# Kernel tuning notes

Measured on AMD Instinct MI355X. Metric: run time of the kernel, lower is better.

## Reference

```python
import jax, jax.numpy as jnp
import numpy as np

DIM = 1024
NUM_HEADS = 16
HEAD_DIM = DIM // NUM_HEADS
SCALE = HEAD_DIM ** -0.5
B, N = 4, 2048


def setup_inputs() -> dict:
    key = jax.random.key(0)
    ks = jax.random.split(key, 5)
    s = 1.0 / np.sqrt(DIM)  # ~ torch Linear init scale
    x = jax.random.normal(ks[0], (B, N, DIM), dtype=jnp.float32)
    Wq = jax.random.normal(ks[1], (DIM, DIM), dtype=jnp.float32) * s
    Wk = jax.random.normal(ks[2], (DIM, DIM), dtype=jnp.float32) * s
    Wv = jax.random.normal(ks[3], (DIM, DIM), dtype=jnp.float32) * s
    Wo = jax.random.normal(ks[4], (DIM, DIM), dtype=jnp.float32) * s
    mask = jnp.tril(jnp.ones((N, N), dtype=bool))  # causal 2D bool mask
    return {"x": x, "mask": mask, "Wq": Wq, "Wk": Wk, "Wv": Wv, "Wo": Wo}


def reference(x, mask, Wq, Wk, Wv, Wo):
    Bb, Nn, D = x.shape
    def split_heads(t):
        return t.reshape(Bb, Nn, NUM_HEADS, HEAD_DIM).transpose(0, 2, 1, 3)  # [B,H,N,d]
    q = split_heads(x @ Wq.T)
    k = split_heads(x @ Wk.T)
    v = split_heads(x @ Wv.T)
    attn = jnp.einsum('bhqd,bhkd->bhqk', q, k) * SCALE  # [B,H,N,N]
    # 2D mask -> broadcast over batch and heads; ~mask positions set to -inf
    attn = jnp.where(mask[None, None, :, :], attn, -jnp.inf)
    attn = jax.nn.softmax(attn, axis=-1)
    out = jnp.einsum('bhqk,bhkd->bhqd', attn, v)
    out = out.transpose(0, 2, 1, 3).reshape(Bb, Nn, D)
    return out @ Wo.T
```

## Files before the change

kernel.cpp:

```cpp
#include <hip/hip_runtime.h>
#include <stdint.h>

#define Bq   4
#define Nseq 2048
#define NH   16
#define HD   64
#define DIMD 1024

typedef float  f32x4   __attribute__((ext_vector_type(4)));
typedef float  f32x16  __attribute__((ext_vector_type(16)));
typedef __bf16 bf16x8  __attribute__((ext_vector_type(8)));
typedef short  s16x4   __attribute__((ext_vector_type(4)));

typedef __attribute__((address_space(1))) void as1_void;
typedef __attribute__((address_space(3))) void as3_void;

static __device__ __forceinline__ uint16_t f2bf(float f) {
    uint32_t u = __builtin_bit_cast(uint32_t, f);
    u += 0x7fffu + ((u >> 16) & 1u);
    return (uint16_t)(u >> 16);
}

static __device__ __forceinline__ uint32_t pk2(float a, float b) {
    uint32_t ua = __builtin_bit_cast(uint32_t, a);
    uint32_t ub = __builtin_bit_cast(uint32_t, b);
    return (ua >> 16) | (ub & 0xffff0000u);
}

static __device__ __forceinline__ void asyncLoad16(const uint16_t* g, uint16_t* l) {
    __builtin_amdgcn_global_load_lds((as1_void*)g, (as3_void*)l, 16, 0, 0);
}

__global__ void cast_all(const float* __restrict__ x,
                         const float* __restrict__ wq, const float* __restrict__ wk,
                         const float* __restrict__ wv, const float* __restrict__ wo,
                         uint16_t* __restrict__ dst) {
    size_t i = ((size_t)blockIdx.x * blockDim.x + threadIdx.x) * 4;
    const float* src; size_t off; float scale = 1.0f;
    if (i < 8388608) { src = x; off = i; }
    else {
        size_t wI = i - 8388608;
        size_t wi = wI >> 20;
        off = wI & 1048575;
        src = (wi == 0) ? wq : (wi == 1) ? wk : (wi == 2) ? wv : wo;
        if (wi == 0) scale = 0.18033688011112042f;
    }
    float4 v = *(const float4*)(src + off);
    ushort4 o;
    o.x = f2bf(v.x * scale); o.y = f2bf(v.y * scale);
    o.z = f2bf(v.z * scale); o.w = f2bf(v.w * scale);
    *(ushort4*)(dst + i) = o;
}

#define BARR()  __builtin_amdgcn_s_barrier()
#define SCB0()  __builtin_amdgcn_sched_barrier(0)
#define LGKM()  asm volatile("s_waitcnt lgkmcnt(0)" ::: "memory")
#define PRIO1() __builtin_amdgcn_s_setprio(1)
#define PRIO0() __builtin_amdgcn_s_setprio(0)

__global__ __launch_bounds__(512, 2) void gemm_qkv384(
    const uint16_t* __restrict__ A, const uint16_t* __restrict__ W0,
    uint16_t* __restrict__ C0, uint16_t* __restrict__ vtb)
{
    __shared__ __align__(16) uint16_t Asm[2][2][4096];
    __shared__ __align__(16) uint16_t Bsm[2][2][12288];

    const int t = threadIdx.x, lane = t & 63, w = t >> 6;
    const int wm = w >> 2, wn = w & 3;
    const int ln = lane & 15, l4 = lane >> 4;

    const int m0 = blockIdx.x * 128;
    const int n0 = blockIdx.y * 384;

    const int srow = t >> 3;
    const int sg   = (t & 7) ^ (srow & 7);
    const uint16_t* aBase = A + (size_t)(m0 + (srow >> 5)*64 + (srow & 31))*DIMD + sg*8;
    const uint16_t* bBase[3];
    #pragma unroll
    for (int j = 0; j < 3; ++j) {
        int f = j*64 + srow;
        int wnf = f / 48, off = f % 48;
        bBase[j] = W0 + (size_t)(n0 + wnf*96 + off)*DIMD + sg*8;
    }

#define SA(mh_, buf_, kk_) asyncLoad16(aBase + (size_t)(mh_)*32*DIMD + (kk_), \
        &Asm[buf_][mh_][t*8])
#define SB(nh_, j_, buf_, kk_) asyncLoad16(bBase[j_] + (size_t)(nh_)*48*DIMD + (kk_), \
        &Bsm[buf_][nh_][(j_)*4096 + t*8])

    SA(0,0,0); SA(1,0,0);
    SB(0,0,0,0); SB(0,1,0,0); SB(0,2,0,0);
    SB(1,0,0,0); SB(1,1,0,0); SB(1,2,0,0);
    SA(0,1,64);
    SB(0,0,1,64); SB(0,1,1,64); SB(0,2,1,64);
    asm volatile("s_waitcnt vmcnt(4)" ::: "memory");
    BARR();

    const int cs0 = ( l4      ^ (ln & 7)) * 8;
    const int cs1 = ((4 + l4) ^ (ln & 7)) * 8;
    const int awo = wm*2048 + ln*64;
    const int bwo = wn*3072 + ln*64;

    bf16x8 af[2][2], bf0[3][2], bf1[3][2];
    f32x4 acc[4][6] = {};

#define LDA(mh_, buf_)                                                         \
    _Pragma("unroll")                                                          \
    for (int mf = 0; mf < 2; ++mf) {                                           \
        af[mf][0] = *(const bf16x8*)(&Asm[buf_][mh_][awo + mf*1024 + cs0]);    \
        af[mf][1] = *(const bf16x8*)(&Asm[buf_][mh_][awo + mf*1024 + cs1]);    \
    }
#define LDB(nh_, buf_, BF)                                                     \
    _Pragma("unroll")                                                          \
    for (int nf = 0; nf < 3; ++nf) {                                           \
        BF[nf][0] = *(const bf16x8*)(&Bsm[buf_][nh_][bwo + nf*1024 + cs0]);    \
        BF[nf][1] = *(const bf16x8*)(&Bsm[buf_][nh_][bwo + nf*1024 + cs1]);    \
    }
#define MFMA12(mh_, nh_, BF)                                                   \
    _Pragma("unroll")                                                          \
    for (int mf = 0; mf < 2; ++mf)                                             \
        _Pragma("unroll")                                                      \
        for (int nf = 0; nf < 3; ++nf) {                                       \
            acc[(mh_)*2+mf][(nh_)*3+nf] = __builtin_amdgcn_mfma_f32_16x16x32_bf16( \
                af[mf][0], BF[nf][0], acc[(mh_)*2+mf][(nh_)*3+nf], 0,0,0);     \
            acc[(mh_)*2+mf][(nh_)*3+nf] = __builtin_amdgcn_mfma_f32_16x16x32_bf16( \
                af[mf][1], BF[nf][1], acc[(mh_)*2+mf][(nh_)*3+nf], 0,0,0);     \
        }

    #pragma unroll 1
    for (int i = 0; i < 8; ++i) {
        const int kk1 = i*128 + 64, kk2 = i*128 + 128, kk3 = i*128 + 192;
        const bool pf = (i < 7);

        LDA(0,0); LDB(0,0,bf0);
        SA(1,1,kk1); SB(1,0,1,kk1);
        BARR(); LGKM(); SCB0();
        PRIO1(); MFMA12(0,0,bf0); PRIO0();
        SCB0(); BARR();

        LDB(1,0,bf1);
        SB(1,1,1,kk1); SB(1,2,1,kk1);
        BARR(); LGKM(); SCB0();
        PRIO1(); MFMA12(0,1,bf1); PRIO0();
        SCB0(); BARR();

        LDA(1,0);
        if (pf) { SA(0,0,kk2); SB(0,0,0,kk2); }
        BARR(); LGKM(); SCB0();
        PRIO1(); MFMA12(1,0,bf0); PRIO0();
        SCB0(); BARR();

        if (pf) { SB(0,1,0,kk2); SB(0,2,0,kk2); }
        BARR(); SCB0();
        PRIO1(); MFMA12(1,1,bf1); PRIO0();
        SCB0();
        if (pf) { asm volatile("s_waitcnt vmcnt(4)" ::: "memory"); }
        else    { asm volatile("s_waitcnt vmcnt(0)" ::: "memory"); }
        BARR();

        LDA(0,1); LDB(0,1,bf0);
        if (pf) { SA(1,0,kk2); SB(1,0,0,kk2); }
        BARR(); LGKM(); SCB0();
        PRIO1(); MFMA12(0,0,bf0); PRIO0();
        SCB0(); BARR();

        LDB(1,1,bf1);
        if (pf) { SB(1,1,0,kk2); SB(1,2,0,kk2); }
        BARR(); LGKM(); SCB0();
        PRIO1(); MFMA12(0,1,bf1); PRIO0();
        SCB0(); BARR();

        LDA(1,1);
        if (pf) { SA(0,1,kk3); SB(0,0,1,kk3); }
        BARR(); LGKM(); SCB0();
        PRIO1(); MFMA12(1,0,bf0); PRIO0();
        SCB0(); BARR();

        if (pf) { SB(0,1,1,kk3); SB(0,2,1,kk3); }
        BARR(); SCB0();
        PRIO1(); MFMA12(1,1,bf1); PRIO0();
        SCB0();
        if (pf) { asm volatile("s_waitcnt vmcnt(4)" ::: "memory"); BARR(); }
    }

#undef SA
#undef SB
#undef LDA
#undef LDB
#undef MFMA12

    #pragma unroll
    for (int mh = 0; mh < 2; ++mh)
      #pragma unroll
      for (int mf = 0; mf < 2; ++mf)
        #pragma unroll
        for (int nh = 0; nh < 2; ++nh)
          #pragma unroll
          for (int nf = 0; nf < 3; ++nf) {
              const f32x4 a4 = acc[mh*2+mf][nh*3+nf];
              int rowg = m0 + wm*64 + mh*32 + mf*16 + l4*4;
              int colg = n0 + wn*96 + nh*48 + nf*16 + ln;
              if (colg < 2048) {
                  uint16_t* C = C0 + (size_t)(colg >> 10) * 8388608;
                  int col = colg & 1023;
                  #pragma unroll
                  for (int r = 0; r < 4; ++r)
                      C[(size_t)(rowg + r)*1024 + col] = f2bf(a4[r]);
              } else {
                  int dg = colg - 2048;
                  int bb = rowg >> 11, nn = rowg & 2047;
                  ushort4 o4;
                  o4.x = f2bf(a4[0]); o4.y = f2bf(a4[1]);
                  o4.z = f2bf(a4[2]); o4.w = f2bf(a4[3]);
                  *(ushort4*)(vtb + ((size_t)(bb*1024 + dg))*Nseq + nn) = o4;
              }
          }
}

__global__ __launch_bounds__(512, 2) void gemm_out256(
    const uint16_t* __restrict__ A, const uint16_t* __restrict__ W0,
    float* __restrict__ C)
{
    __shared__ __align__(16) uint16_t Asm[2][2][8192];
    __shared__ __align__(16) uint16_t Bsm[2][2][4096];

    const int t = threadIdx.x, lane = t & 63, w = t >> 6;
    const int wm = w >> 2, wn = w & 3;
    const int ln = lane & 15, l4 = lane >> 4;

    const int m0 = blockIdx.x * 256;
    const int n0 = blockIdx.y * 128;

    const int srow = t >> 3;
    const int sg   = (t & 7) ^ (srow & 7);
    const uint16_t* aBase = A + (size_t)(m0 + srow)*DIMD + sg*8;
    const uint16_t* bBase = W0 + (size_t)(n0 + (srow >> 4)*32 + (srow & 15))*DIMD + sg*8;

#define SA(mh_, j_, buf_, kk_) asyncLoad16(aBase + (size_t)((j_)*128 + (mh_)*64)*DIMD + (kk_), \
        &Asm[buf_][mh_][(j_)*4096 + t*8])
#define SB(nh_, buf_, kk_) asyncLoad16(bBase + (size_t)(nh_)*16*DIMD + (kk_), \
        &Bsm[buf_][nh_][t*8])

    SB(0,0,0); SB(1,0,0);
    SA(0,0,0,0); SA(0,1,0,0);
    SA(1,0,0,0); SA(1,1,0,0);
    SB(0,1,64); SB(1,1,64);
    SA(0,0,1,64); SA(0,1,1,64);
    asm volatile("s_waitcnt vmcnt(4)" ::: "memory");
    BARR();

    const int cs0 = ( l4      ^ (ln & 7)) * 8;
    const int cs1 = ((4 + l4) ^ (ln & 7)) * 8;
    const int awo = wm*4096 + ln*64;
    const int bwo = wn*1024 + ln*64;

    bf16x8 af[4][2], bfA[2], bfB[2];
    f32x4 acc[8][2] = {};

#define LDA(mh_, buf_)                                                         \
    _Pragma("unroll")                                                          \
    for (int mf = 0; mf < 4; ++mf) {                                           \
        af[mf][0] = *(const bf16x8*)(&Asm[buf_][mh_][awo + mf*1024 + cs0]);    \
        af[mf][1] = *(const bf16x8*)(&Asm[buf_][mh_][awo + mf*1024 + cs1]);    \
    }
#define LDB(nh_, buf_, BF)                                                     \
    BF[0] = *(const bf16x8*)(&Bsm[buf_][nh_][bwo + cs0]);                      \
    BF[1] = *(const bf16x8*)(&Bsm[buf_][nh_][bwo + cs1]);
#define MFMA8(mh_, nh_, BF)                                                    \
    _Pragma("unroll")                                                          \
    for (int mf = 0; mf < 4; ++mf) {                                           \
        acc[(mh_)*4+mf][nh_] = __builtin_amdgcn_mfma_f32_16x16x32_bf16(        \
            af[mf][0], BF[0], acc[(mh_)*4+mf][nh_], 0,0,0);                    \
        acc[(mh_)*4+mf][nh_] = __builtin_amdgcn_mfma_f32_16x16x32_bf16(        \
            af[mf][1], BF[1], acc[(mh_)*4+mf][nh_], 0,0,0);                    \
    }

    #pragma unroll 1
    for (int i = 0; i < 8; ++i) {
        const int kk1 = i*128 + 64, kk2 = i*128 + 128, kk3 = i*128 + 192;
        const bool pf2 = (i < 7);
        const bool pf3 = (i < 7);

        LDA(0,0); LDB(0,0,bfA);
        SA(1,0,1,kk1); SA(1,1,1,kk1);
        BARR(); LGKM(); SCB0();
        PRIO1(); MFMA8(0,0,bfA); PRIO0();
        SCB0(); BARR();

        LDB(1,0,bfB);
        BARR(); LGKM(); SCB0();
        PRIO1(); MFMA8(0,1,bfB); PRIO0();
        SCB0(); BARR();

        LDA(1,0);
        if (pf2) { SB(0,0,kk2); SB(1,0,kk2); SA(0,0,0,kk2); SA(0,1,0,kk2); }
        BARR(); LGKM(); SCB0();
        PRIO1(); MFMA8(1,0,bfA); PRIO0();
        SCB0(); BARR();

        BARR(); SCB0();
        PRIO1(); MFMA8(1,1,bfB); PRIO0();
        SCB0();
        if (pf2) { asm volatile("s_waitcnt vmcnt(4)" ::: "memory"); }
        else     { asm volatile("s_waitcnt vmcnt(0)" ::: "memory"); }
        BARR();

        LDA(0,1); LDB(0,1,bfA);
        if (pf2) { SA(1,0,0,kk2); SA(1,1,0,kk2); }
        BARR(); LGKM(); SCB0();
        PRIO1(); MFMA8(0,0,bfA); PRIO0();
        SCB0(); BARR();

        LDB(1,1,bfB);
        BARR(); LGKM(); SCB0();
        PRIO1(); MFMA8(0,1,bfB); PRIO0();
        SCB0(); BARR();

        LDA(1,1);
        if (pf3) { SB(0,1,kk3); SB(1,1,kk3); SA(0,0,1,kk3); SA(0,1,1,kk3); }
        BARR(); LGKM(); SCB0();
        PRIO1(); MFMA8(1,0,bfA); PRIO0();
        SCB0(); BARR();

        BARR(); SCB0();
        PRIO1(); MFMA8(1,1,bfB); PRIO0();
        SCB0();
        if (pf3) { asm volatile("s_waitcnt vmcnt(4)" ::: "memory"); BARR(); }
    }

#undef SA
#undef SB
#undef LDA
#undef LDB
#undef MFMA8

    #pragma unroll
    for (int mh = 0; mh < 2; ++mh)
      #pragma unroll
      for (int mf = 0; mf < 4; ++mf)
        #pragma unroll
        for (int nh = 0; nh < 2; ++nh) {
            const f32x4 a4 = acc[mh*4+mf][nh];
            int rowg = m0 + wm*128 + mh*64 + mf*16 + l4*4;
            int colg = n0 + wn*32 + nh*16 + ln;
            #pragma unroll
            for (int r = 0; r < 4; ++r)
                C[(size_t)(rowg + r)*1024 + colg] = a4[r];
        }
}

__global__ __launch_bounds__(256, 3) void attn(
    const uint16_t* __restrict__ Q, const uint16_t* __restrict__ K,
    const uint16_t* __restrict__ Vt, uint16_t* __restrict__ O)
{
    __shared__ __align__(16) uint16_t Kb[3][64*64];
    __shared__ __align__(16) uint16_t Vb[3][64*64];

    const int t = threadIdx.x, lane = t & 63, w = t >> 6;
    const int quad = lane >> 4, c = lane & 15;
    const int y = blockIdx.y;
    const int qi = (y < 4) ? (15 - y) : (y < 8) ? (y + 4) : (y < 12) ? (y - 4) : (15 - y);
    const int q0 = qi * 128;
    const int bh = blockIdx.x, b = bh >> 4, h = bh & 15;
    const size_t tokBase = (size_t)b * Nseq;
    const int hcol = h * HD;
    uint16_t* Qs = (uint16_t*)Kb;

    #define STAGE_KV(k0_, buf_)                                             \
        _Pragma("unroll")                                                    \
        for (int i = 0; i < 2; ++i) {                                        \
            int s = t + 256*i;                                               \
            int row = s >> 3, gg = (s & 7) ^ (row & 7);                      \
            asyncLoad16(K + (tokBase + (k0_) + row)*DIMD + hcol + gg*8,      \
                        Kb[buf_] + (size_t)(w*64 + 256*i)*8);                \
            asyncLoad16(Vt + ((size_t)bh*HD + row)*Nseq + (k0_) + gg*8,      \
                        Vb[buf_] + (size_t)(w*64 + 256*i)*8);                \
        }

    #pragma unroll
    for (int i = 0; i < 4; ++i) {
        int s = t + 256*i;
        int row = s >> 3, gg = (s & 7) ^ (row & 7);
        asyncLoad16(Q + (tokBase + q0 + row)*DIMD + hcol + gg*8,
                    Qs + (size_t)(w*64 + 256*i)*8);
    }
    __syncthreads();
    bf16x8 qf[2][2];
    #pragma unroll
    for (int qt = 0; qt < 2; ++qt)
        #pragma unroll
        for (int ks = 0; ks < 2; ++ks) {
            int row = w*32 + qt*16 + c;
            int pos = (ks*4 + quad) ^ (row & 7);
            qf[qt][ks] = *(const bf16x8*)(Qs + (size_t)(row*8 + pos)*8);
        }
    __syncthreads();

    const int wrow0 = q0 + w*32;
    const int end = 2*qi + 2;
    STAGE_KV(0, 0);
    STAGE_KV(64, 1);

    f32x4  o[2][4] = {};
    float  l_lane[2] = {0.f, 0.f};
    int b0 = 0, b1 = 1, b2 = 2;

    for (int kt = 0; kt < end; ++kt) {
        const int k0 = kt * 64;

        if (kt + 1 < end) { asm volatile("s_waitcnt vmcnt(4)\n\ts_barrier" ::: "memory"); }
        else              { asm volatile("s_waitcnt vmcnt(0)\n\ts_barrier" ::: "memory"); }

        if (kt + 2 < end) { STAGE_KV((kt+2)*64, b2); }

        if (k0 <= wrow0 + 31) {
            const uint16_t* Ks = Kb[b0];
            const uint16_t* Vs = Vb[b0];

            f32x4 sv[2][4] = {};
            __builtin_amdgcn_s_setprio(1);
            #pragma unroll
            for (int nt = 0; nt < 4; ++nt)
                #pragma unroll
                for (int ks = 0; ks < 2; ++ks) {
                    int row = nt*16 + c;
                    int pos = (ks*4 + quad) ^ (row & 7);
                    bf16x8 kf = *(const bf16x8*)(Ks + (size_t)(row*8 + pos)*8);
                    sv[0][nt] = __builtin_amdgcn_mfma_f32_16x16x32_bf16(kf, qf[0][ks], sv[0][nt], 0, 0, 0);
                    sv[1][nt] = __builtin_amdgcn_mfma_f32_16x16x32_bf16(kf, qf[1][ks], sv[1][nt], 0, 0, 0);
                }
            __builtin_amdgcn_s_setprio(0);

            if (k0 + 63 > wrow0) {
                #pragma unroll
                for (int qt = 0; qt < 2; ++qt)
                    #pragma unroll
                    for (int nt = 0; nt < 4; ++nt)
                        #pragma unroll
                        for (int r = 0; r < 4; ++r) {
                            int kvg = k0 + nt*16 + quad*4 + r;
                            int qg  = wrow0 + qt*16 + c;
                            if (kvg > qg) sv[qt][nt][r] = -340.0f;
                        }
            }

            s16x4 pb[2][4];
            #pragma unroll
            for (int qt = 0; qt < 2; ++qt)
                #pragma unroll
                for (int nt = 0; nt < 4; ++nt) {
                    float p0 = __builtin_amdgcn_exp2f(sv[qt][nt][0]);
                    float p1 = __builtin_amdgcn_exp2f(sv[qt][nt][1]);
                    float p2 = __builtin_amdgcn_exp2f(sv[qt][nt][2]);
                    float p3 = __builtin_amdgcn_exp2f(sv[qt][nt][3]);
                    l_lane[qt] += (p0 + p1) + (p2 + p3);
                    union { uint32_t u[2]; s16x4 v; } pu;
                    pu.u[0] = pk2(p0, p1);
                    pu.u[1] = pk2(p2, p3);
                    pb[qt][nt] = pu.v;
                }

            __builtin_amdgcn_s_setprio(1);
            #pragma unroll
            for (int s4 = 0; s4 < 4; ++s4)
                #pragma unroll
                for (int dt = 0; dt < 4; ++dt) {
                    int row = dt*16 + c;
                    int chunk = s4*2 + (quad >> 1);
                    int pos = chunk ^ (row & 7);
                    s16x4 vf = *(const s16x4*)(Vs + (size_t)(row*8 + pos)*8 + (quad & 1)*4);
                    o[0][dt] = __builtin_amdgcn_mfma_f32_16x16x16bf16_1k(vf, pb[0][s4], o[0][dt], 0, 0, 0);
                    o[1][dt] = __builtin_amdgcn_mfma_f32_16x16x16bf16_1k(vf, pb[1][s4], o[1][dt], 0, 0, 0);
                }
            __builtin_amdgcn_s_setprio(0);
        }

        int tmp = b0; b0 = b1; b1 = b2; b2 = tmp;
    }

    #pragma unroll
    for (int qt = 0; qt < 2; ++qt) {
        float l = l_lane[qt];
        l += __shfl_xor(l, 16);
        l += __shfl_xor(l, 32);
        float inv = 1.0f / l;
        int tok = (int)(q0 + w*32 + qt*16 + c);
        #pragma unroll
        for (int dt = 0; dt < 4; ++dt) {
            ushort4 o4;
            o4.x = f2bf(o[qt][dt][0] * inv);
            o4.y = f2bf(o[qt][dt][1] * inv);
            o4.z = f2bf(o[qt][dt][2] * inv);
            o4.w = f2bf(o[qt][dt][3] * inv);
            *(ushort4*)(O + (tokBase + tok)*DIMD + hcol + dt*16 + quad*4) = o4;
        }
    }
    #undef STAGE_KV
}

extern "C" void kernel_launch(void* const* d_in, const int* in_sizes, int n_in,
                              void* d_out, int out_size, void* d_ws, size_t ws_size,
                              hipStream_t stream) {
    const float* x  = (const float*)d_in[0];
    const float* Wq = (const float*)d_in[2];
    const float* Wk = (const float*)d_in[3];
    const float* Wv = (const float*)d_in[4];
    const float* Wo = (const float*)d_in[5];

    uint16_t* ws  = (uint16_t*)d_ws;
    uint16_t* xb  = ws;
    uint16_t* wqb = ws + 8388608;
    uint16_t* wob = wqb + 3*1048576;
    uint16_t* qb  = ws + 12582912;
    uint16_t* kb  = qb + 8388608;
    uint16_t* vtb = kb + 8388608;
    uint16_t* ab  = xb;

    cast_all<<<12288, 256, 0, stream>>>(x, Wq, Wk, Wv, Wo, ws);

    gemm_qkv384<<<dim3(64, 8), 512, 0, stream>>>(xb, wqb, qb, vtb);

    attn<<<dim3(64, 16), 256, 0, stream>>>(qb, kb, vtb, ab);

    gemm_out256<<<dim3(32, 8), 512, 0, stream>>>(ab, wob, (float*)d_out);
}
```

Baseline: 242.8 us.

## Software-pipeline QK^T/softmax of next KV tile with PV of current tile

```diff
diff --git a/kernel.cpp b/kernel.cpp
--- a/kernel.cpp
+++ b/kernel.cpp
@@ -397,85 +397,94 @@
     __syncthreads();
 
     const int wrow0 = q0 + w*32;
-    const int end = 2*qi + 2;
+    const int end   = 2*qi + 2;
+    const int lastw = (wrow0 + 31) >> 6;
     STAGE_KV(0, 0);
     STAGE_KV(64, 1);
 
     f32x4  o[2][4] = {};
     float  l_lane[2] = {0.f, 0.f};
+    s16x4  pbA[2][4], pbB[2][4];
+
+    #define QKSM(j_, PB, KSP)                                                  \
+    {                                                                          \
+        const uint16_t* Ks_ = (KSP);                                           \
+        const int k0_ = (j_) * 64;                                             \
+        f32x4 sv[2][4] = {};                                                   \
+        __builtin_amdgcn_s_setprio(1);                                         \
+        _Pragma("unroll")                                                      \
+        for (int nt = 0; nt < 4; ++nt)                                         \
+            _Pragma("unroll")                                                  \
+            for (int ks = 0; ks < 2; ++ks) {                                   \
+                int row = nt*16 + c;                                           \
+                int pos = (ks*4 + quad) ^ (row & 7);                           \
+                bf16x8 kf = *(const bf16x8*)(Ks_ + (size_t)(row*8 + pos)*8);   \
+                sv[0][nt] = __builtin_amdgcn_mfma_f32_16x16x32_bf16(kf, qf[0][ks], sv[0][nt], 0,0,0); \
+                sv[1][nt] = __builtin_amdgcn_mfma_f32_16x16x32_bf16(kf, qf[1][ks], sv[1][nt], 0,0,0); \
+            }                                                                  \
+        __builtin_amdgcn_s_setprio(0);                                         \
+        if (k0_ + 63 > wrow0) {                                                \
+            _Pragma("unroll")                                                  \
+            for (int qt = 0; qt < 2; ++qt)                                     \
+                _Pragma("unroll")                                              \
+                for (int nt = 0; nt < 4; ++nt)                                 \
+                    _Pragma("unroll")                                          \
+                    for (int r = 0; r < 4; ++r) {                              \
+                        int kvg = k0_ + nt*16 + quad*4 + r;                    \
+                        int qg  = wrow0 + qt*16 + c;                           \
+                        if (kvg > qg) sv[qt][nt][r] = -340.0f;                 \
+                    }                                                          \
+        }                                                                      \
+        _Pragma("unroll")                                                      \
+        for (int qt = 0; qt < 2; ++qt)                                         \
+            _Pragma("unroll")                                                  \
+            for (int nt = 0; nt < 4; ++nt) {                                   \
+                float p0 = __builtin_amdgcn_exp2f(sv[qt][nt][0]);              \
+                float p1 = __builtin_amdgcn_exp2f(sv[qt][nt][1]);              \
+                float p2 = __builtin_amdgcn_exp2f(sv[qt][nt][2]);              \
+                float p3 = __builtin_amdgcn_exp2f(sv[qt][nt][3]);              \
+                l_lane[qt] += (p0 + p1) + (p2 + p3);                           \
+                union { uint32_t u[2]; s16x4 v; } pu;                          \
+                pu.u[0] = pk2(p0, p1);                                         \
+                pu.u[1] = pk2(p2, p3);                                         \
+                PB[qt][nt] = pu.v;                                             \
+            }                                                                  \
+    }
+
+    #define PVOP(PB, VSP)                                                      \
+    {                                                                          \
+        const uint16_t* Vs_ = (VSP);                                           \
+        __builtin_amdgcn_s_setprio(1);                                         \
+        _Pragma("unroll")                                                      \
+        for (int s4 = 0; s4 < 4; ++s4)                                         \
+            _Pragma("unroll")                                                  \
+            for (int dt = 0; dt < 4; ++dt) {                                   \
+                int row = dt*16 + c;                                           \
+                int chunk = s4*2 + (quad >> 1);                                \
+                int pos = chunk ^ (row & 7);                                   \
+                s16x4 vf = *(const s16x4*)(Vs_ + (size_t)(row*8 + pos)*8 + (quad & 1)*4); \
+                o[0][dt] = __builtin_amdgcn_mfma_f32_16x16x16bf16_1k(vf, PB[0][s4], o[0][dt], 0,0,0); \
+                o[1][dt] = __builtin_amdgcn_mfma_f32_16x16x16bf16_1k(vf, PB[1][s4], o[1][dt], 0,0,0); \
+            }                                                                  \
+        __builtin_amdgcn_s_setprio(0);                                         \
+    }
+
+    asm volatile("s_waitcnt vmcnt(4)\n\ts_barrier" ::: "memory");
+    QKSM(0, pbA, Kb[0]);
+
     int b0 = 0, b1 = 1, b2 = 2;
-
-    for (int kt = 0; kt < end; ++kt) {
-        const int k0 = kt * 64;
-
-        if (kt + 1 < end) { asm volatile("s_waitcnt vmcnt(4)\n\ts_barrier" ::: "memory"); }
-        else              { asm volatile("s_waitcnt vmcnt(0)\n\ts_barrier" ::: "memory"); }
-
+    for (int kt = 0; kt < end; kt += 2) {
+        asm volatile("s_waitcnt vmcnt(0)\n\ts_barrier" ::: "memory");
         if (kt + 2 < end) { STAGE_KV((kt+2)*64, b2); }
-
-        if (k0 <= wrow0 + 31) {
-            const uint16_t* Ks = Kb[b0];
-            const uint16_t* Vs = Vb[b0];
-
-            f32x4 sv[2][4] = {};
-            __builtin_amdgcn_s_setprio(1);
-            #pragma unroll
-            for (int nt = 0; nt < 4; ++nt)
-                #pragma unroll
-                for (int ks = 0; ks < 2; ++ks) {
-                    int row = nt*16 + c;
-                    int pos = (ks*4 + quad) ^ (row & 7);
-                    bf16x8 kf = *(const bf16x8*)(Ks + (size_t)(row*8 + pos)*8);
-                    sv[0][nt] = __builtin_amdgcn_mfma_f32_16x16x32_bf16(kf, qf[0][ks], sv[0][nt], 0, 0, 0);
-                    sv[1][nt] = __builtin_amdgcn_mfma_f32_16x16x32_bf16(kf, qf[1][ks], sv[1][nt], 0, 0, 0);
-                }
-            __builtin_amdgcn_s_setprio(0);
-
-            if (k0 + 63 > wrow0) {
-                #pragma unroll
-                for (int qt = 0; qt < 2; ++qt)
-                    #pragma unroll
-                    for (int nt = 0; nt < 4; ++nt)
-                        #pragma unroll
-                        for (int r = 0; r < 4; ++r) {
-                            int kvg = k0 + nt*16 + quad*4 + r;
-                            int qg  = wrow0 + qt*16 + c;
-                            if (kvg > qg) sv[qt][nt][r] = -340.0f;
-                        }
-            }
-
-            s16x4 pb[2][4];
-            #pragma unroll
-            for (int qt = 0; qt < 2; ++qt)
-                #pragma unroll
-                for (int nt = 0; nt < 4; ++nt) {
-                    float p0 = __builtin_amdgcn_exp2f(sv[qt][nt][0]);
-                    float p1 = __builtin_amdgcn_exp2f(sv[qt][nt][1]);
-                    float p2 = __builtin_amdgcn_exp2f(sv[qt][nt][2]);
-                    float p3 = __builtin_amdgcn_exp2f(sv[qt][nt][3]);
-                    l_lane[qt] += (p0 + p1) + (p2 + p3);
-                    union { uint32_t u[2]; s16x4 v; } pu;
-                    pu.u[0] = pk2(p0, p1);
-                    pu.u[1] = pk2(p2, p3);
-                    pb[qt][nt] = pu.v;
-                }
-
-            __builtin_amdgcn_s_setprio(1);
-            #pragma unroll
-            for (int s4 = 0; s4 < 4; ++s4)
-                #pragma unroll
-                for (int dt = 0; dt < 4; ++dt) {
-                    int row = dt*16 + c;
-                    int chunk = s4*2 + (quad >> 1);
-                    int pos = chunk ^ (row & 7);
-                    s16x4 vf = *(const s16x4*)(Vs + (size_t)(row*8 + pos)*8 + (quad & 1)*4);
-                    o[0][dt] = __builtin_amdgcn_mfma_f32_16x16x16bf16_1k(vf, pb[0][s4], o[0][dt], 0, 0, 0);
-                    o[1][dt] = __builtin_amdgcn_mfma_f32_16x16x16bf16_1k(vf, pb[1][s4], o[1][dt], 0, 0, 0);
-                }
-            __builtin_amdgcn_s_setprio(0);
-        }
-
-        int tmp = b0; b0 = b1; b1 = b2; b2 = tmp;
+        if (kt + 1 <= lastw) { QKSM(kt+1, pbB, Kb[b1]); }
+        if (kt     <= lastw) { PVOP(pbA, Vb[b0]); }
+        { int tmp = b0; b0 = b1; b1 = b2; b2 = tmp; }
+
+        asm volatile("s_waitcnt vmcnt(0)\n\ts_barrier" ::: "memory");
+        if (kt + 3 < end) { STAGE_KV((kt+3)*64, b2); }
+        if (kt + 2 <= lastw) { QKSM(kt+2, pbA, Kb[b1]); }
+        if (kt + 1 <= lastw) { PVOP(pbB, Vb[b0]); }
+        { int tmp = b0; b0 = b1; b1 = b2; b2 = tmp; }
     }
 
     #pragma unroll
@@ -496,6 +505,8 @@
         }
     }
     #undef STAGE_KV
+    #undef QKSM
+    #undef PVOP
 }
 
 extern "C" void kernel_launch(void* const* d_in, const int* in_sizes, int n_in,
```

New measurement: 241.3 us, median of 3. Within noise of the previous version (-0.6%).
